# Optimization experiments

Measured on AMD Instinct MI355X. Metric: run time of the kernel, lower is better.

Reference implementation:

```python
import jax, jax.numpy as jnp
import numpy as np

B, T, D, H, K, ED = 4, 1024, 512, 8, 30, 128
HD = D // H
SCALE = HD ** -0.5


def _ln(x, g, b, eps=1e-5):
    m = jnp.mean(x, axis=-1, keepdims=True)
    v = jnp.var(x, axis=-1, keepdims=True)
    return (x - m) / jnp.sqrt(v + eps) * g + b


def setup_inputs() -> dict:
    key = jax.random.key(0)
    ks = jax.random.split(key, 16)
    s = 0.02
    return {
        "h_V": jax.random.normal(ks[0], (B, T, D), jnp.float32),
        "k": jax.random.normal(ks[1], (B, T, D), jnp.float32),
        "v": jax.random.normal(ks[2], (B, T, D), jnp.float32),
        "E": jax.random.normal(ks[3], (B, T, K, ED), jnp.float32),
        "bias": jax.random.normal(ks[4], (B, T, T), jnp.float32),
        "Wq": jax.random.normal(ks[5], (D, D), jnp.float32) * s,
        "bq": jnp.zeros((D,), jnp.float32),
        "Wk": jax.random.normal(ks[6], (D, D), jnp.float32) * s,
        "bk": jnp.zeros((D,), jnp.float32),
        "Wv": jax.random.normal(ks[7], (D, D), jnp.float32) * s,
        "bv": jnp.zeros((D,), jnp.float32),
        "Wo": jax.random.normal(ks[8], (D, D + ED), jnp.float32) * s,
        "bo": jnp.zeros((D,), jnp.float32),
        "t": jax.random.normal(ks[9], (1,), jnp.float32),
        "gn": jnp.ones((D,), jnp.float32),
        "bn": jnp.zeros((D,), jnp.float32),
        "w1": jax.random.normal(ks[10], (4 * D, D), jnp.float32) * s,
        "bw1": jnp.zeros((4 * D,), jnp.float32),
        "w2": jax.random.normal(ks[11], (D, 4 * D), jnp.float32) * s,
        "bw2": jnp.zeros((D,), jnp.float32),
        "gf": jnp.ones((D,), jnp.float32),
        "bf": jnp.zeros((D,), jnp.float32),
        "g2": jnp.ones((D,), jnp.float32),
        "b2": jnp.zeros((D,), jnp.float32),
        "E_idx": jax.random.randint(ks[12], (B, T, K), 0, T),
        "mask": jax.random.randint(ks[13], (B, T), 0, 2).astype(jnp.int32),
    }


def reference(h_V, k, v, E, bias, Wq, bq, Wk, bk, Wv, bv, Wo, bo, t, gn, bn, w1, bw1, w2, bw2, gf, bf, g2, b2, E_idx, mask):
    # q/k/v projections; q scaled by head_dim**-0.5 (as in torch: q *= scaling)
    q = (h_V @ Wq.T + bq) * SCALE
    kk = k @ Wk.T + bk
    vv = v @ Wv.T + bv
    qh = q.reshape(B, T, H, HD)
    kh = kk.reshape(B, T, H, HD)
    vh = vv.reshape(B, T, H, HD)
    # attention logits with additive pairwise bias, broadcast over heads
    aw = jnp.einsum('bthd,bshd->bhts', qh, kh) + bias[:, None, :, :]
    aw = jnp.where(mask[:, None, None, :] == 0, -1e9, aw)
    # h_attend temperature scaling
    aw = aw / (4.0 ** jnp.tanh(t[0]))
    p = jax.nn.softmax(aw, axis=-1)  # [B,H,T,S]
    attn = jnp.einsum('bhts,bshd->bthd', p, vh).reshape(B, T, D)
    # edge path: head-mean attention, gather neighbor weights, weighted edge sum
    ma = jnp.mean(p, axis=1)                       # [B,T,S]
    g = jnp.take_along_axis(ma, E_idx, axis=-1)    # [B,T,K]
    edge = (g[..., None] * E).sum(axis=2) / (g.sum(axis=-1, keepdims=True) + 1e-6)  # [B,T,ED]
    out = jnp.concatenate([attn, edge], axis=-1) @ Wo.T + bo
    h = _ln(h_V + out, gn, bn, eps=1e-5)
    # PositionwiseFeedForward: residual + LN(eps=1e-6)
    ff = jax.nn.gelu(h @ w1.T + bw1, approximate=False) @ w2.T + bw2
    dh = _ln(h + ff, gf, bf, eps=1e-6)
    return _ln(h + dh, g2, b2, eps=1e-5)
```

## Files before the change

kernel.cpp:

```cpp
#include <hip/hip_runtime.h>
#include <hip/hip_fp16.h>
#include <math.h>

#define B_ 4
#define T_ 1024
#define D_ 512
#define H_ 8
#define HD_ 64
#define KN 30
#define ED_ 128
#define DFF_ 2048
#define M_ 4096
#define BH_ 32

typedef _Float16 f16;
typedef __attribute__((ext_vector_type(8))) _Float16 f16x8;
typedef __attribute__((ext_vector_type(4))) _Float16 f16x4;
typedef __attribute__((ext_vector_type(4))) float f32x4;

#define MFMA16 __builtin_amdgcn_mfma_f32_16x16x32_f16
#define LOG2E 1.44269504088896f

__device__ __forceinline__ f16x8 ld8(const f16* p){ return *reinterpret_cast<const f16x8*>(p); }

__device__ __forceinline__ void gld16(const void* g, void* l){
  __builtin_amdgcn_global_load_lds((const __attribute__((address_space(1))) void*)g,
                                   (__attribute__((address_space(3))) void*)l, 16, 0, 0);
}

struct CvtJobs {
  const float* s[9];
  f16* d[9];
  int start[10];
};

__global__ __launch_bounds__(256) void prep_kernel(
    CvtJobs J, int cvtBlocks,
    const float* __restrict__ bias, const int* __restrict__ mask,
    const float* __restrict__ tsc, f16* __restrict__ biasT)
{
  if (blockIdx.x < cvtBlocks){
    const int blk = blockIdx.x;
    int j = 0;
    while (j < 8 && blk >= J.start[j+1]) ++j;
    const int i = (blk - J.start[j])*256 + threadIdx.x;
    float4 v = reinterpret_cast<const float4*>(J.s[j])[i];
    union { f16 h[4]; ushort4 u; } o;
    o.h[0]=(f16)v.x; o.h[1]=(f16)v.y; o.h[2]=(f16)v.z; o.h[3]=(f16)v.w;
    reinterpret_cast<ushort4*>(J.d[j])[i] = o.u;
    return;
  }
  const int u = (blockIdx.x - cvtBlocks)*256 + threadIdx.x;
  const int l4 = u & 3, l16 = (u >> 2) & 15, qg = (u >> 6) & 1;
  const int ws = (u >> 7) & 3, c = (u >> 9) & 7, tb = (u >> 12) & 31, bi = u >> 17;
  const float s = exp2f(-2.0f*tanhf(tsc[0]))*LOG2E;
  const int t  = tb*32 + qg*16 + l16;
  const int s0 = c*128 + ws*32 + l4*4;
  const float* bp = bias + ((size_t)bi*T_ + t)*T_ + s0;
  const int*   mp = mask + bi*T_ + s0;
  union { f16 h[8]; f16x8 v8; } o;
#pragma unroll
  for (int st = 0; st < 2; ++st){
    float4 v = *reinterpret_cast<const float4*>(bp + st*16);
    int4  mm = *reinterpret_cast<const int4*>(mp + st*16);
    float x[4] = {v.x,v.y,v.z,v.w};
    int  m4[4] = {mm.x,mm.y,mm.z,mm.w};
#pragma unroll
    for (int j = 0; j < 4; ++j){
      float tv = (x[j] + (m4[j] ? 0.f : -60000.f))*s;
      o.h[st*4 + j] = (f16)fmaxf(tv, -60000.f);
    }
  }
  *reinterpret_cast<f16x8*>(biasT + (size_t)u*8) = o.v8;
}

template<int EPI>
__global__ __launch_bounds__(256,2) void gemm_tile(
    const f16* __restrict__ X, const f16* __restrict__ W,
    const float* __restrict__ bias, void* __restrict__ outp,
    int Kd, int ldo, int nbN)
{
  __shared__ f16 As[128*64];
  __shared__ f16 Bs[128*64];
  const int nwg = gridDim.x;
  const int bid = blockIdx.x;
  const int swz = (bid & 7)*(nwg >> 3) + (bid >> 3);
  const int mb = swz / nbN, nb = swz - mb*nbN;
  const int rb = mb*128, cb = nb*128;
  const int tid = threadIdx.x;
  const int w = tid >> 6, lane = tid & 63;
  const int l16 = lane & 15, l4 = lane >> 4;
  const int wr = w >> 1, wc = w & 1;
  const int key = l16 & 7;

  f32x4 acc[4][4];
#pragma unroll
  for (int m = 0; m < 4; ++m)
#pragma unroll
    for (int n = 0; n < 4; ++n) acc[m][n] = (f32x4){0.f,0.f,0.f,0.f};

  for (int k0 = 0; k0 < Kd; k0 += 64){
#pragma unroll
    for (int i = 0; i < 4; ++i){
      const int cidx = i*256 + w*64 + lane;
      const int r = cidx >> 3, p = cidx & 7;
      gld16(X + (size_t)(rb + r)*Kd + k0 + ((p ^ (r & 7)) << 3),
            &As[(i*256 + w*64)*8]);
      gld16(W + (size_t)(cb + r)*Kd + k0 + ((p ^ (r & 7)) << 3),
            &Bs[(i*256 + w*64)*8]);
    }
    __syncthreads();
#pragma unroll
    for (int kk = 0; kk < 2; ++kk){
      f16x8 a[4], b[4];
#pragma unroll
      for (int m = 0; m < 4; ++m)
        a[m] = ld8(&As[(wr*64 + m*16 + l16)*64 + (((kk*4 + l4) ^ key) << 3)]);
#pragma unroll
      for (int n = 0; n < 4; ++n)
        b[n] = ld8(&Bs[(wc*64 + n*16 + l16)*64 + (((kk*4 + l4) ^ key) << 3)]);
#pragma unroll
      for (int m = 0; m < 4; ++m)
#pragma unroll
        for (int n = 0; n < 4; ++n)
          acc[m][n] = MFMA16(a[m], b[n], acc[m][n], 0,0,0);
    }
    __syncthreads();
  }

#pragma unroll
  for (int n = 0; n < 4; ++n){
    const int col = cb + wc*64 + n*16 + l16;
    const float bv = bias[col];
#pragma unroll
    for (int m = 0; m < 4; ++m){
#pragma unroll
      for (int j = 0; j < 4; ++j){
        const int row = rb + wr*64 + m*16 + l4*4 + j;
        float v = acc[m][n][j] + bv;
        if (EPI == 1) v = 0.5f*v*(1.0f + erff(v*0.70710678118654752f));
        ((f16*)outp)[(size_t)row*ldo + col] = (f16)v;
      }
    }
  }
}

template<int EPI>
__global__ __launch_bounds__(256,2) void gemm_n64(
    const f16* __restrict__ X, const f16* __restrict__ W,
    const float* __restrict__ bias, void* __restrict__ outp,
    int Kd, int ldo, int nbN)
{
  __shared__ f16 As[128*64];
  __shared__ f16 Bs[64*64];
  const int nwg = gridDim.x;
  const int bid = blockIdx.x;
  const int swz = (bid & 7)*(nwg >> 3) + (bid >> 3);
  const int mb = swz / nbN, nb = swz - mb*nbN;
  const int rb = mb*128, cb = nb*64;
  const int tid = threadIdx.x;
  const int w = tid >> 6, lane = tid & 63;
  const int l16 = lane & 15, l4 = lane >> 4;
  const int wr = w >> 1, wc = w & 1;
  const int key = l16 & 7;

  f32x4 acc[4][2];
#pragma unroll
  for (int m = 0; m < 4; ++m)
#pragma unroll
    for (int n = 0; n < 2; ++n) acc[m][n] = (f32x4){0.f,0.f,0.f,0.f};

  for (int k0 = 0; k0 < Kd; k0 += 64){
#pragma unroll
    for (int i = 0; i < 4; ++i){
      const int cidx = i*256 + w*64 + lane;
      const int r = cidx >> 3, p = cidx & 7;
      gld16(X + (size_t)(rb + r)*Kd + k0 + ((p ^ (r & 7)) << 3),
            &As[(i*256 + w*64)*8]);
    }
#pragma unroll
    for (int i = 0; i < 2; ++i){
      const int cidx = i*256 + w*64 + lane;
      const int r = cidx >> 3, p = cidx & 7;
      gld16(W + (size_t)(cb + r)*Kd + k0 + ((p ^ (r & 7)) << 3),
            &Bs[(i*256 + w*64)*8]);
    }
    __syncthreads();
#pragma unroll
    for (int kk = 0; kk < 2; ++kk){
      f16x8 a[4], b[2];
#pragma unroll
      for (int m = 0; m < 4; ++m)
        a[m] = ld8(&As[(wr*64 + m*16 + l16)*64 + (((kk*4 + l4) ^ key) << 3)]);
#pragma unroll
      for (int n = 0; n < 2; ++n)
        b[n] = ld8(&Bs[(wc*32 + n*16 + l16)*64 + (((kk*4 + l4) ^ key) << 3)]);
#pragma unroll
      for (int m = 0; m < 4; ++m)
#pragma unroll
        for (int n = 0; n < 2; ++n)
          acc[m][n] = MFMA16(a[m], b[n], acc[m][n], 0,0,0);
    }
    __syncthreads();
  }

#pragma unroll
  for (int n = 0; n < 2; ++n){
    const int col = cb + wc*32 + n*16 + l16;
    const float bv = bias[col];
#pragma unroll
    for (int m = 0; m < 4; ++m){
#pragma unroll
      for (int j = 0; j < 4; ++j){
        const int row = rb + wr*64 + m*16 + l4*4 + j;
        float v = acc[m][n][j] + bv;
        if (EPI == 1) v = 0.5f*v*(1.0f + erff(v*0.70710678118654752f));
        ((f16*)outp)[(size_t)row*ldo + col] = (f16)v;
      }
    }
  }
}

__global__ __launch_bounds__(256,2) void qkv_tile(
    const f16* __restrict__ hV, const f16* __restrict__ kI, const f16* __restrict__ vI,
    const f16* __restrict__ Wq, const f16* __restrict__ Wk, const f16* __restrict__ Wv,
    const float* __restrict__ bq, const float* __restrict__ bk, const float* __restrict__ bv,
    const float* __restrict__ tsc,
    f16* __restrict__ qo, f16* __restrict__ ko, f16* __restrict__ vT)
{
  __shared__ f16 As[128*64];
  __shared__ f16 Bs[128*64];
  const int bid = blockIdx.x;
  const int swz = (bid & 7)*48 + (bid >> 3);
  const int g = swz >> 7;
  const int r = swz & 127;
  const int mb = r >> 2, nb = r & 3;
  const f16* X  = (g == 0) ? hV : ((g == 1) ? kI : vI);
  const f16* W  = (g == 0) ? Wq : ((g == 1) ? Wk : Wv);
  const float* bias = (g == 0) ? bq : ((g == 1) ? bk : bv);
  const int rb = mb*128, cb = nb*128;
  const int tid = threadIdx.x;
  const int w = tid >> 6, lane = tid & 63;
  const int l16 = lane & 15, l4 = lane >> 4;
  const int wr = w >> 1, wc = w & 1;
  const int key = l16 & 7;

  f32x4 acc[4][4];
#pragma unroll
  for (int m = 0; m < 4; ++m)
#pragma unroll
    for (int n = 0; n < 4; ++n) acc[m][n] = (f32x4){0.f,0.f,0.f,0.f};

  for (int k0 = 0; k0 < D_; k0 += 64){
#pragma unroll
    for (int i = 0; i < 4; ++i){
      const int cidx = i*256 + w*64 + lane;
      const int rr = cidx >> 3, p = cidx & 7;
      gld16(X + (size_t)(rb + rr)*D_ + k0 + ((p ^ (rr & 7)) << 3),
            &As[(i*256 + w*64)*8]);
      gld16(W + (size_t)(cb + rr)*D_ + k0 + ((p ^ (rr & 7)) << 3),
            &Bs[(i*256 + w*64)*8]);
    }
    __syncthreads();
#pragma unroll
    for (int kk = 0; kk < 2; ++kk){
      f16x8 a[4], b[4];
#pragma unroll
      for (int m = 0; m < 4; ++m)
        a[m] = ld8(&As[(wr*64 + m*16 + l16)*64 + (((kk*4 + l4) ^ key) << 3)]);
#pragma unroll
      for (int n = 0; n < 4; ++n)
        b[n] = ld8(&Bs[(wc*64 + n*16 + l16)*64 + (((kk*4 + l4) ^ key) << 3)]);
#pragma unroll
      for (int m = 0; m < 4; ++m)
#pragma unroll
        for (int n = 0; n < 4; ++n)
          acc[m][n] = MFMA16(a[m], b[n], acc[m][n], 0,0,0);
    }
    __syncthreads();
  }

  const float qs = exp2f(-2.0f*tanhf(tsc[0]))*LOG2E*0.125f;
  const float scale = (g == 0) ? qs : 1.0f;
  f16* out = (g == 0) ? qo : ko;
#pragma unroll
  for (int n = 0; n < 4; ++n){
    const int col = cb + wc*64 + n*16 + l16;
    const float bv = bias[col];
#pragma unroll
    for (int m = 0; m < 4; ++m){
#pragma unroll
      for (int j = 0; j < 4; ++j){
        const int row = rb + wr*64 + m*16 + l4*4 + j;
        const float v = (acc[m][n][j] + bv)*scale;
        if (g < 2){
          out[(size_t)row*D_ + col] = (f16)v;
        } else {
          const int b = row >> 10, t = row & (T_-1);
          const int h = col >> 6,  dl = col & (HD_-1);
          vT[(((size_t)b*H_ + h)*HD_ + dl)*T_ + t] = (f16)v;
        }
      }
    }
  }
}

__global__ __launch_bounds__(512,4) void attn_fused(
    const f16* __restrict__ q, const f16* __restrict__ k, const f16* __restrict__ vT,
    const f16* __restrict__ biasT, const int* __restrict__ eidx,
    f16* __restrict__ X2, float* __restrict__ gpart)
{
  __shared__ f16 Sb[16384];
  __shared__ f16 Pc[32*128];
  const int bid = blockIdx.x;
  const int swz = (bid & 7)*128 + (bid >> 3);
  const int bh = swz >> 5, tb = swz & 31;
  const int bi = bh >> 3, h = bh & 7;
  const int t0 = tb*32;
  const int tid = threadIdx.x, w = tid >> 6, lane = tid & 63;
  const int qg = w >> 2, ws = w & 3;
  const int l16 = lane & 15, l4 = lane >> 4;
  const int key = l16 & 7;

  const f16* qp = q + (size_t)(bi*T_ + t0 + qg*16 + l16)*D_ + h*HD_ + l4*8;
  const f16x8 q0 = ld8(qp), q1 = ld8(qp + 32);
  const f16* bb = biasT + (size_t)(bi*32 + tb)*32768 + ws*1024 + qg*512 + l16*32 + l4*8;
  f16x8 bfr[8];
#pragma unroll
  for (int c = 0; c < 8; ++c) bfr[c] = ld8(bb + c*4096);
  const int tl = tid & 255;
  int ga_r, ga_kk, ga_id, gb_r = 0, gb_kk = 0, gb_id = -1;
  ga_r = tl/KN; ga_kk = tl - ga_r*KN;
  ga_id = eidx[((size_t)(bi*T_ + t0 + qg*16 + ga_r))*KN + ga_kk];
  if (tl + 256 < 16*KN){
    gb_r = (tl+256)/KN; gb_kk = (tl+256) - gb_r*KN;
    gb_id = eidx[((size_t)(bi*T_ + t0 + qg*16 + gb_r))*KN + gb_kk];
  }

  const f16* kg = k + (size_t)(bi*T_)*D_ + h*HD_;
  const f16* vg = vT + (size_t)bh*HD_*T_;

  auto stageK = [&](int c, int slot){
#pragma unroll
    for (int i = 0; i < 2; ++i){
      const int cidx = i*512 + w*64 + lane;
      const int r = cidx >> 3, p = cidx & 7;
      gld16(kg + (size_t)(c*128 + r)*D_ + ((p ^ (r & 7)) << 3),
            &Sb[slot*8192 + (i*512 + w*64)*8]);
    }
  };
  auto stageV = [&](int sc, int slot){
#pragma unroll
    for (int i = 0; i < 2; ++i){
      const int cidx = i*512 + w*64 + lane;
      const int r = cidx >> 4, p = cidx & 15;
      gld16(vg + (size_t)r*T_ + sc*128 + ((p ^ (r & 7)) << 3),
            &Sb[slot*8192 + (i*512 + w*64)*8]);
    }
  };

  f32x4 acc[16];
  stageK(0, 0);
#pragma unroll
  for (int c = 0; c < 8; ++c){
    if (c < 7) stageK(c+1, (c+1)&1);
    if (c < 7) asm volatile("s_waitcnt vmcnt(2)" ::: "memory");
    else       asm volatile("s_waitcnt vmcnt(0)" ::: "memory");
    __builtin_amdgcn_sched_barrier(0);
    __builtin_amdgcn_s_barrier();
    __builtin_amdgcn_sched_barrier(0);
    const int base = (c&1)*8192;
#pragma unroll
    for (int step = 0; step < 2; ++step){
      const int rr = ws*32 + step*16 + l16;
      f32x4 a = {0.f,0.f,0.f,0.f};
      a = MFMA16(ld8(&Sb[base + rr*64 + ((l4 ^ key) << 3)]),       q0, a, 0,0,0);
      a = MFMA16(ld8(&Sb[base + rr*64 + (((4 + l4) ^ key) << 3)]), q1, a, 0,0,0);
#pragma unroll
      for (int j = 0; j < 4; ++j) a[j] += (float)bfr[c][step*4 + j];
      acc[c*2 + step] = a;
    }
    __builtin_amdgcn_s_barrier();
  }

  float* redf = (float*)Sb;
  float m = -3.4e38f;
#pragma unroll
  for (int c = 0; c < 16; ++c)
#pragma unroll
    for (int j = 0; j < 4; ++j) m = fmaxf(m, acc[c][j]);
  m = fmaxf(m, __shfl_xor(m, 16));
  m = fmaxf(m, __shfl_xor(m, 32));
  if (lane < 16) redf[(qg*4 + ws)*16 + lane] = m;
  __syncthreads();
  m = fmaxf(fmaxf(redf[(qg*4+0)*16 + l16], redf[(qg*4+1)*16 + l16]),
            fmaxf(redf[(qg*4+2)*16 + l16], redf[(qg*4+3)*16 + l16]));
  float l = 0.f;
#pragma unroll
  for (int c = 0; c < 16; ++c)
#pragma unroll
    for (int j = 0; j < 4; ++j){
      const float e = exp2f(acc[c][j] - m);
      l += e;
      acc[c][j] = e;
    }
  l += __shfl_xor(l, 16);
  l += __shfl_xor(l, 32);
  if (lane < 16) redf[128 + (qg*4 + ws)*16 + lane] = l;
  __syncthreads();
  const float lrq = redf[128 + (qg*4+0)*16 + l16] + redf[128 + (qg*4+1)*16 + l16]
                  + redf[128 + (qg*4+2)*16 + l16] + redf[128 + (qg*4+3)*16 + l16];
  __syncthreads();
  const float lr_a = __shfl(lrq, ga_r);
  const float lr_b = __shfl(lrq, gb_r);

  f32x4 oo0 = {0.f,0.f,0.f,0.f}, oo1 = oo0, oo2 = oo0, oo3 = oo0;
  float pva = 0.f, pvb = 0.f;
  stageV(0, 0);
#pragma unroll
  for (int sc = 0; sc < 8; ++sc){
#pragma unroll
    for (int step = 0; step < 2; ++step){
      const int slb = ws*32 + step*16 + l4*4;
      f16x4 pp;
#pragma unroll
      for (int j = 0; j < 4; ++j) pp[j] = (f16)acc[sc*2 + step][j];
      *reinterpret_cast<f16x4*>(
          &Pc[(qg*16 + l16)*128 + (((slb >> 3) ^ key) << 3) + (slb & 7)]) = pp;
    }
    if (sc < 7) stageV(sc+1, (sc+1)&1);
    if (sc < 7) asm volatile("s_waitcnt vmcnt(2) lgkmcnt(0)" ::: "memory");
    else        asm volatile("s_waitcnt vmcnt(0) lgkmcnt(0)" ::: "memory");
    __builtin_amdgcn_sched_barrier(0);
    __builtin_amdgcn_s_barrier();
    __builtin_amdgcn_sched_barrier(0);
    const int base = (sc&1)*8192;
    const int vrow = (ws*16 + l16)*128;
#pragma unroll
    for (int grp = 0; grp < 4; ++grp){
      const int ch = (grp*4 + l4) ^ key;
      const f16x8 pa = ld8(&Pc[(qg*16 + l16)*128 + (ch << 3)]);
      const f16x8 vb = ld8(&Sb[base + vrow + (ch << 3)]);
      if (grp == 0)      oo0 = MFMA16(pa, vb, oo0, 0,0,0);
      else if (grp == 1) oo1 = MFMA16(pa, vb, oo1, 0,0,0);
      else if (grp == 2) oo2 = MFMA16(pa, vb, oo2, 0,0,0);
      else               oo3 = MFMA16(pa, vb, oo3, 0,0,0);
    }
    if ((ga_id >> 7) == sc){
      const int r = qg*16 + ga_r;
      const int sl = ga_id & 127;
      pva = (float)Pc[r*128 + ((((sl >> 3) ^ (r & 7)) << 3) | (sl & 7))];
    }
    if (gb_id >= 0 && (gb_id >> 7) == sc){
      const int r = qg*16 + gb_r;
      const int sl = gb_id & 127;
      pvb = (float)Pc[r*128 + ((((sl >> 3) ^ (r & 7)) << 3) | (sl & 7))];
    }
    __builtin_amdgcn_s_barrier();
  }
  const f32x4 o = (oo0 + oo1) + (oo2 + oo3);

  gpart[((size_t)bh*T_ + t0 + qg*16 + ga_r)*KN + ga_kk] = pva/lr_a*0.125f;
  if (gb_id >= 0)
    gpart[((size_t)bh*T_ + t0 + qg*16 + gb_r)*KN + gb_kk] = pvb/lr_b*0.125f;

#pragma unroll
  for (int j = 0; j < 4; ++j){
    const float lr = __shfl(lrq, l4*4 + j);
    const int t = t0 + qg*16 + l4*4 + j;
    X2[((size_t)(bi*T_ + t))*640 + h*HD_ + ws*16 + l16] = (f16)(o[j]/lr);
  }
}

__global__ __launch_bounds__(128) void edge_kernel(
    const float* __restrict__ gpart, const float* __restrict__ E, f16* __restrict__ X2)
{
  __shared__ float gl[KN];
  __shared__ float ginv;
  const int bt = blockIdx.x;
  const int bi = bt >> 10, tt = bt & 1023;
  const int t = threadIdx.x;
  if (t < KN){
    float s = 0.f;
#pragma unroll
    for (int hh = 0; hh < H_; ++hh)
      s += gpart[((size_t)(bi*H_ + hh)*T_ + tt)*KN + t];
    gl[t] = s;
  }
  __syncthreads();
  if (t == 0){
    float s = 0.f;
#pragma unroll
    for (int i = 0; i < KN; ++i) s += gl[i];
    ginv = 1.0f/(s + 1e-6f);
  }
  __syncthreads();
  float acc = 0.f;
  const float* Ep = E + (size_t)bt*KN*ED_ + t;
#pragma unroll 5
  for (int kk = 0; kk < KN; ++kk) acc += gl[kk]*Ep[(size_t)kk*ED_];
  X2[(size_t)bt*640 + 512 + t] = (f16)(acc*ginv);
}

__device__ __forceinline__ float block_sum(float v, float* sbuf){
  for (int o = 32; o; o >>= 1) v += __shfl_down(v, o);
  __syncthreads();
  if ((threadIdx.x & 63) == 0) sbuf[threadIdx.x >> 6] = v;
  __syncthreads();
  return sbuf[0]+sbuf[1]+sbuf[2]+sbuf[3];
}

__global__ __launch_bounds__(256) void ln1_kernel(
    const float* __restrict__ hV, const f16* __restrict__ hraw,
    const float* __restrict__ gn, const float* __restrict__ bn,
    f16* __restrict__ hh)
{
  __shared__ float sbuf[4];
  const int r = blockIdx.x, t = threadIdx.x;
  const size_t base = (size_t)r*D_;
  float x0 = hV[base+t]     + (float)hraw[base+t];
  float x1 = hV[base+t+256] + (float)hraw[base+t+256];
  float s = block_sum(x0+x1, sbuf);
  const float mean = s*(1.f/512.f);
  float d0 = x0-mean, d1 = x1-mean;
  float vs = block_sum(d0*d0+d1*d1, sbuf);
  const float rstd = rsqrtf(vs*(1.f/512.f) + 1e-5f);
  hh[base+t]     = (f16)(d0*rstd*gn[t]     + bn[t]);
  hh[base+t+256] = (f16)(d1*rstd*gn[t+256] + bn[t+256]);
}

__global__ __launch_bounds__(256) void final_kernel(
    const f16* __restrict__ hh, const f16* __restrict__ ffr,
    const float* __restrict__ gf, const float* __restrict__ bfv,
    const float* __restrict__ g2, const float* __restrict__ b2,
    float* __restrict__ out)
{
  __shared__ float sbuf[4];
  const int r = blockIdx.x, t = threadIdx.x;
  const size_t base = (size_t)r*D_;
  const float h0 = (float)hh[base+t], h1 = (float)hh[base+t+256];
  float x0 = h0 + (float)ffr[base+t], x1 = h1 + (float)ffr[base+t+256];
  float s = block_sum(x0+x1, sbuf);
  float mean = s*(1.f/512.f);
  float d0 = x0-mean, d1 = x1-mean;
  float vs = block_sum(d0*d0+d1*d1, sbuf);
  float rstd = rsqrtf(vs*(1.f/512.f) + 1e-6f);
  const float dh0 = d0*rstd*gf[t]     + bfv[t];
  const float dh1 = d1*rstd*gf[t+256] + bfv[t+256];
  const float y0 = h0 + dh0, y1 = h1 + dh1;
  s = block_sum(y0+y1, sbuf);
  mean = s*(1.f/512.f);
  d0 = y0-mean; d1 = y1-mean;
  vs = block_sum(d0*d0+d1*d1, sbuf);
  rstd = rsqrtf(vs*(1.f/512.f) + 1e-5f);
  out[base+t]     = d0*rstd*g2[t]     + b2[t];
  out[base+t+256] = d1*rstd*g2[t+256] + b2[t+256];
}

extern "C" void kernel_launch(void* const* d_in, const int* in_sizes, int n_in,
                              void* d_out, int out_size, void* d_ws, size_t ws_size,
                              hipStream_t stream)
{
  (void)in_sizes; (void)n_in; (void)out_size;
  const float* h_V  = (const float*)d_in[0];
  const float* kin  = (const float*)d_in[1];
  const float* vin  = (const float*)d_in[2];
  const float* E    = (const float*)d_in[3];
  const float* bias = (const float*)d_in[4];
  const float* Wq   = (const float*)d_in[5];
  const float* bq   = (const float*)d_in[6];
  const float* Wk   = (const float*)d_in[7];
  const float* bk   = (const float*)d_in[8];
  const float* Wv   = (const float*)d_in[9];
  const float* bv   = (const float*)d_in[10];
  const float* Wo   = (const float*)d_in[11];
  const float* bo   = (const float*)d_in[12];
  const float* tsc  = (const float*)d_in[13];
  const float* gn   = (const float*)d_in[14];
  const float* bn   = (const float*)d_in[15];
  const float* w1   = (const float*)d_in[16];
  const float* bw1  = (const float*)d_in[17];
  const float* w2   = (const float*)d_in[18];
  const float* bw2  = (const float*)d_in[19];
  const float* gf   = (const float*)d_in[20];
  const float* bfv  = (const float*)d_in[21];
  const float* g2   = (const float*)d_in[22];
  const float* b2   = (const float*)d_in[23];
  const int*   Eidx = (const int*)d_in[24];
  const int*   mask = (const int*)d_in[25];
  float* out = (float*)d_out;

  char* wsb = (char*)d_ws;
  size_t off = 0;
  auto alloc = [&](size_t bytes) -> void* {
    void* pp = wsb + off; off += (bytes + 255) & ~(size_t)255; return pp;
  };
  f16* hVb  = (f16*)alloc((size_t)M_*D_*2);
  f16* kbI  = (f16*)alloc((size_t)M_*D_*2);
  f16* vbI  = (f16*)alloc((size_t)M_*D_*2);
  f16* Wqb  = (f16*)alloc((size_t)D_*D_*2);
  f16* Wkb  = (f16*)alloc((size_t)D_*D_*2);
  f16* Wvb  = (f16*)alloc((size_t)D_*D_*2);
  f16* Wob  = (f16*)alloc((size_t)D_*(D_+ED_)*2);
  f16* w1b  = (f16*)alloc((size_t)DFF_*D_*2);
  f16* w2b  = (f16*)alloc((size_t)D_*DFF_*2);
  f16* qb   = (f16*)alloc((size_t)M_*D_*2);
  f16* kb   = (f16*)alloc((size_t)M_*D_*2);
  f16* vT   = (f16*)alloc((size_t)M_*D_*2);
  f16* biasT= (f16*)alloc((size_t)B_*T_*T_*2);
  f16* X2   = (f16*)alloc((size_t)M_*640*2);
  float* gpart = (float*)alloc((size_t)BH_*T_*KN*4);
  f16* hraw = (f16*)alloc((size_t)M_*D_*2);
  f16* hh   = (f16*)alloc((size_t)M_*D_*2);
  f16* ff1  = (f16*)alloc((size_t)M_*DFF_*2);
  if (ws_size < off) return;
  f16* ffraw = hraw;

  {
    CvtJobs J;
    const float* srcs[9] = {h_V, kin, vin, Wq, Wk, Wv, Wo, w1, w2};
    f16* dsts[9] = {hVb, kbI, vbI, Wqb, Wkb, Wvb, Wob, w1b, w2b};
    const int n4s[9] = {M_*D_/4, M_*D_/4, M_*D_/4, D_*D_/4, D_*D_/4, D_*D_/4,
                        D_*(D_+ED_)/4, DFF_*D_/4, D_*DFF_/4};
    int cum = 0;
    for (int i = 0; i < 9; ++i){
      J.s[i] = srcs[i]; J.d[i] = dsts[i]; J.start[i] = cum;
      cum += n4s[i]/256;
    }
    J.start[9] = cum;
    prep_kernel<<<cum + 2048,256,0,stream>>>(J, cum, bias, mask, tsc, biasT);
  }

  qkv_tile<<<384,256,0,stream>>>(hVb, kbI, vbI, Wqb, Wkb, Wvb, bq, bk, bv, tsc, qb, kb, vT);

  attn_fused<<<1024,512,0,stream>>>(qb, kb, vT, biasT, Eidx, X2, gpart);

  edge_kernel<<<M_,128,0,stream>>>(gpart, E, X2);

  gemm_n64<2><<<256,256,0,stream>>>(X2, Wob, bo, hraw, D_+ED_, D_, 8);
  ln1_kernel<<<M_,256,0,stream>>>(h_V, hraw, gn, bn, hh);

  gemm_tile<1><<<512,256,0,stream>>>(hh, w1b, bw1, ff1, D_, DFF_, 16);
  gemm_n64<2><<<256,256,0,stream>>>(ff1, w2b, bw2, ffraw, DFF_, D_, 8);

  final_kernel<<<M_,256,0,stream>>>(hh, ffraw, gf, bfv, g2, b2, out);
}
```

Baseline: 159.3 us.

## Double-buffer LDS tiles in GEMM kernels to overlap global loads with MFMA

Adds a two-slot LDS ring to the three GEMM kernels (gemm_tile, gemm_n64, qkv_tile). Each iteration issues the next k-phase's direct-to-LDS loads before computing the current one, and waits with vmcnt counters so only the older batch must have landed. This is meant to hide global load latency behind MFMA work. LDS use per block doubles (64KB for the 128x128 kernels), which may lower occupancy; gemm_n64 also raises its launch_bounds hint to 3 blocks.

Result: no change. 156.7 us (-1.6%).

```diff
diff --git a/kernel.cpp b/kernel.cpp
--- a/kernel.cpp
+++ b/kernel.cpp
@@ -80,8 +80,8 @@
     const float* __restrict__ bias, void* __restrict__ outp,
     int Kd, int ldo, int nbN)
 {
-  __shared__ f16 As[128*64];
-  __shared__ f16 Bs[128*64];
+  __shared__ f16 As[2*8192];
+  __shared__ f16 Bs[2*8192];
   const int nwg = gridDim.x;
   const int bid = blockIdx.x;
   const int swz = (bid & 7)*(nwg >> 3) + (bid >> 3);
@@ -93,39 +93,50 @@
   const int wr = w >> 1, wc = w & 1;
   const int key = l16 & 7;
 
-  f32x4 acc[4][4];
-#pragma unroll
-  for (int m = 0; m < 4; ++m)
-#pragma unroll
-    for (int n = 0; n < 4; ++n) acc[m][n] = (f32x4){0.f,0.f,0.f,0.f};
-
-  for (int k0 = 0; k0 < Kd; k0 += 64){
+  auto stage = [&](int ph, int slot){
 #pragma unroll
     for (int i = 0; i < 4; ++i){
       const int cidx = i*256 + w*64 + lane;
       const int r = cidx >> 3, p = cidx & 7;
-      gld16(X + (size_t)(rb + r)*Kd + k0 + ((p ^ (r & 7)) << 3),
-            &As[(i*256 + w*64)*8]);
-      gld16(W + (size_t)(cb + r)*Kd + k0 + ((p ^ (r & 7)) << 3),
-            &Bs[(i*256 + w*64)*8]);
-    }
-    __syncthreads();
+      gld16(X + (size_t)(rb + r)*Kd + ph*64 + ((p ^ (r & 7)) << 3),
+            &As[slot*8192 + (i*256 + w*64)*8]);
+      gld16(W + (size_t)(cb + r)*Kd + ph*64 + ((p ^ (r & 7)) << 3),
+            &Bs[slot*8192 + (i*256 + w*64)*8]);
+    }
+  };
+
+  f32x4 acc[4][4];
+#pragma unroll
+  for (int m = 0; m < 4; ++m)
+#pragma unroll
+    for (int n = 0; n < 4; ++n) acc[m][n] = (f32x4){0.f,0.f,0.f,0.f};
+
+  const int nPh = Kd >> 6;
+  stage(0, 0);
+  for (int ph = 0; ph < nPh; ++ph){
+    if (ph < nPh-1) stage(ph+1, (ph+1)&1);
+    if (ph < nPh-1) asm volatile("s_waitcnt vmcnt(8)" ::: "memory");
+    else            asm volatile("s_waitcnt vmcnt(0)" ::: "memory");
+    __builtin_amdgcn_sched_barrier(0);
+    __builtin_amdgcn_s_barrier();
+    __builtin_amdgcn_sched_barrier(0);
+    const int base = (ph&1)*8192;
 #pragma unroll
     for (int kk = 0; kk < 2; ++kk){
       f16x8 a[4], b[4];
 #pragma unroll
       for (int m = 0; m < 4; ++m)
-        a[m] = ld8(&As[(wr*64 + m*16 + l16)*64 + (((kk*4 + l4) ^ key) << 3)]);
+        a[m] = ld8(&As[base + (wr*64 + m*16 + l16)*64 + (((kk*4 + l4) ^ key) << 3)]);
 #pragma unroll
       for (int n = 0; n < 4; ++n)
-        b[n] = ld8(&Bs[(wc*64 + n*16 + l16)*64 + (((kk*4 + l4) ^ key) << 3)]);
+        b[n] = ld8(&Bs[base + (wc*64 + n*16 + l16)*64 + (((kk*4 + l4) ^ key) << 3)]);
 #pragma unroll
       for (int m = 0; m < 4; ++m)
 #pragma unroll
         for (int n = 0; n < 4; ++n)
           acc[m][n] = MFMA16(a[m], b[n], acc[m][n], 0,0,0);
     }
-    __syncthreads();
+    __builtin_amdgcn_s_barrier();
   }
 
 #pragma unroll
@@ -146,13 +157,13 @@
 }
 
 template<int EPI>
-__global__ __launch_bounds__(256,2) void gemm_n64(
+__global__ __launch_bounds__(256,3) void gemm_n64(
     const f16* __restrict__ X, const f16* __restrict__ W,
     const float* __restrict__ bias, void* __restrict__ outp,
     int Kd, int ldo, int nbN)
 {
-  __shared__ f16 As[128*64];
-  __shared__ f16 Bs[64*64];
+  __shared__ f16 As[2*8192];
+  __shared__ f16 Bs[2*4096];
   const int nwg = gridDim.x;
   const int bid = blockIdx.x;
   const int swz = (bid & 7)*(nwg >> 3) + (bid >> 3);
@@ -164,44 +175,55 @@
   const int wr = w >> 1, wc = w & 1;
   const int key = l16 & 7;
 
-  f32x4 acc[4][2];
-#pragma unroll
-  for (int m = 0; m < 4; ++m)
-#pragma unroll
-    for (int n = 0; n < 2; ++n) acc[m][n] = (f32x4){0.f,0.f,0.f,0.f};
-
-  for (int k0 = 0; k0 < Kd; k0 += 64){
+  auto stage = [&](int ph, int slot){
 #pragma unroll
     for (int i = 0; i < 4; ++i){
       const int cidx = i*256 + w*64 + lane;
       const int r = cidx >> 3, p = cidx & 7;
-      gld16(X + (size_t)(rb + r)*Kd + k0 + ((p ^ (r & 7)) << 3),
-            &As[(i*256 + w*64)*8]);
+      gld16(X + (size_t)(rb + r)*Kd + ph*64 + ((p ^ (r & 7)) << 3),
+            &As[slot*8192 + (i*256 + w*64)*8]);
     }
 #pragma unroll
     for (int i = 0; i < 2; ++i){
       const int cidx = i*256 + w*64 + lane;
       const int r = cidx >> 3, p = cidx & 7;
-      gld16(W + (size_t)(cb + r)*Kd + k0 + ((p ^ (r & 7)) << 3),
-            &Bs[(i*256 + w*64)*8]);
-    }
-    __syncthreads();
+      gld16(W + (size_t)(cb + r)*Kd + ph*64 + ((p ^ (r & 7)) << 3),
+            &Bs[slot*4096 + (i*256 + w*64)*8]);
+    }
+  };
+
+  f32x4 acc[4][2];
+#pragma unroll
+  for (int m = 0; m < 4; ++m)
+#pragma unroll
+    for (int n = 0; n < 2; ++n) acc[m][n] = (f32x4){0.f,0.f,0.f,0.f};
+
+  const int nPh = Kd >> 6;
+  stage(0, 0);
+  for (int ph = 0; ph < nPh; ++ph){
+    if (ph < nPh-1) stage(ph+1, (ph+1)&1);
+    if (ph < nPh-1) asm volatile("s_waitcnt vmcnt(6)" ::: "memory");
+    else            asm volatile("s_waitcnt vmcnt(0)" ::: "memory");
+    __builtin_amdgcn_sched_barrier(0);
+    __builtin_amdgcn_s_barrier();
+    __builtin_amdgcn_sched_barrier(0);
+    const int baseA = (ph&1)*8192, baseB = (ph&1)*4096;
 #pragma unroll
     for (int kk = 0; kk < 2; ++kk){
       f16x8 a[4], b[2];
 #pragma unroll
       for (int m = 0; m < 4; ++m)
-        a[m] = ld8(&As[(wr*64 + m*16 + l16)*64 + (((kk*4 + l4) ^ key) << 3)]);
+        a[m] = ld8(&As[baseA + (wr*64 + m*16 + l16)*64 + (((kk*4 + l4) ^ key) << 3)]);
 #pragma unroll
       for (int n = 0; n < 2; ++n)
-        b[n] = ld8(&Bs[(wc*32 + n*16 + l16)*64 + (((kk*4 + l4) ^ key) << 3)]);
+        b[n] = ld8(&Bs[baseB + (wc*32 + n*16 + l16)*64 + (((kk*4 + l4) ^ key) << 3)]);
 #pragma unroll
       for (int m = 0; m < 4; ++m)
 #pragma unroll
         for (int n = 0; n < 2; ++n)
           acc[m][n] = MFMA16(a[m], b[n], acc[m][n], 0,0,0);
     }
-    __syncthreads();
+    __builtin_amdgcn_s_barrier();
   }
 
 #pragma unroll
@@ -228,8 +250,8 @@
     const float* __restrict__ tsc,
     f16* __restrict__ qo, f16* __restrict__ ko, f16* __restrict__ vT)
 {
-  __shared__ f16 As[128*64];
-  __shared__ f16 Bs[128*64];
+  __shared__ f16 As[2*8192];
+  __shared__ f16 Bs[2*8192];
   const int bid = blockIdx.x;
   const int swz = (bid & 7)*48 + (bid >> 3);
   const int g = swz >> 7;
@@ -245,39 +267,50 @@
   const int wr = w >> 1, wc = w & 1;
   const int key = l16 & 7;
 
-  f32x4 acc[4][4];
-#pragma unroll
-  for (int m = 0; m < 4; ++m)
-#pragma unroll
-    for (int n = 0; n < 4; ++n) acc[m][n] = (f32x4){0.f,0.f,0.f,0.f};
-
-  for (int k0 = 0; k0 < D_; k0 += 64){
+  auto stage = [&](int ph, int slot){
 #pragma unroll
     for (int i = 0; i < 4; ++i){
       const int cidx = i*256 + w*64 + lane;
       const int rr = cidx >> 3, p = cidx & 7;
-      gld16(X + (size_t)(rb + rr)*D_ + k0 + ((p ^ (rr & 7)) << 3),
-            &As[(i*256 + w*64)*8]);
-      gld16(W + (size_t)(cb + rr)*D_ + k0 + ((p ^ (rr & 7)) << 3),
-            &Bs[(i*256 + w*64)*8]);
-    }
-    __syncthreads();
+      gld16(X + (size_t)(rb + rr)*D_ + ph*64 + ((p ^ (rr & 7)) << 3),
+            &As[slot*8192 + (i*256 + w*64)*8]);
+      gld16(W + (size_t)(cb + rr)*D_ + ph*64 + ((p ^ (rr & 7)) << 3),
+            &Bs[slot*8192 + (i*256 + w*64)*8]);
+    }
+  };
+
+  f32x4 acc[4][4];
+#pragma unroll
+  for (int m = 0; m < 4; ++m)
+#pragma unroll
+    for (int n = 0; n < 4; ++n) acc[m][n] = (f32x4){0.f,0.f,0.f,0.f};
+
+  stage(0, 0);
+#pragma unroll
+  for (int ph = 0; ph < 8; ++ph){
+    if (ph < 7) stage(ph+1, (ph+1)&1);
+    if (ph < 7) asm volatile("s_waitcnt vmcnt(8)" ::: "memory");
+    else        asm volatile("s_waitcnt vmcnt(0)" ::: "memory");
+    __builtin_amdgcn_sched_barrier(0);
+    __builtin_amdgcn_s_barrier();
+    __builtin_amdgcn_sched_barrier(0);
+    const int base = (ph&1)*8192;
 #pragma unroll
     for (int kk = 0; kk < 2; ++kk){
       f16x8 a[4], b[4];
 #pragma unroll
       for (int m = 0; m < 4; ++m)
-        a[m] = ld8(&As[(wr*64 + m*16 + l16)*64 + (((kk*4 + l4) ^ key) << 3)]);
+        a[m] = ld8(&As[base + (wr*64 + m*16 + l16)*64 + (((kk*4 + l4) ^ key) << 3)]);
 #pragma unroll
       for (int n = 0; n < 4; ++n)
-        b[n] = ld8(&Bs[(wc*64 + n*16 + l16)*64 + (((kk*4 + l4) ^ key) << 3)]);
+        b[n] = ld8(&Bs[base + (wc*64 + n*16 + l16)*64 + (((kk*4 + l4) ^ key) << 3)]);
 #pragma unroll
       for (int m = 0; m < 4; ++m)
 #pragma unroll
         for (int n = 0; n < 4; ++n)
           acc[m][n] = MFMA16(a[m], b[n], acc[m][n], 0,0,0);
     }
-    __syncthreads();
+    __builtin_amdgcn_s_barrier();
   }
 
   const float qs = exp2f(-2.0f*tanhf(tsc[0]))*LOG2E*0.125f;
```
